# Optimization experiments

Hardware: AMD Instinct MI355X
Metric: run time of the kernel (lower is better)

Reference implementation:

```python
import jax, jax.numpy as jnp
import numpy as np

EPS = 1e-8

def setup_inputs() -> dict:
    key = jax.random.key(0)
    ks = jax.random.split(key, 12)
    bsz, input_dim, output_dim = 65536, 512, 512
    base_mem_size, category_mem_size, mem_dim, n_cat = 100, 5, 64, 35
    def kaiming(k, shape):
        fan_in = shape[-1]
        bound = np.sqrt(6.0 / fan_in)  # kaiming_uniform with a=sqrt(5) default gain approximated by gain=1 uniform: sqrt(6/fan_in)
        return jax.random.uniform(k, shape, jnp.float32, -bound, bound)
    def linear(kw, kb, out_d, in_d):
        bound = 1.0 / np.sqrt(in_d)
        W = jax.random.uniform(kw, (out_d, in_d), jnp.float32, -bound, bound)
        b = jax.random.uniform(kb, (out_d,), jnp.float32, -bound, bound)
        return W, b
    W_base, b_base = linear(ks[0], ks[1], mem_dim, input_dim)
    W_cat, b_cat = linear(ks[2], ks[3], mem_dim, input_dim)
    W_out, b_out = linear(ks[4], ks[5], output_dim, 2 * mem_dim)
    base_keys = kaiming(ks[6], (base_mem_size, mem_dim))
    base_vals = kaiming(ks[7], (base_mem_size, mem_dim))
    cat_keys = kaiming(ks[8], (n_cat, category_mem_size, mem_dim))
    cat_vals = kaiming(ks[9], (n_cat, category_mem_size, mem_dim))
    query = jax.random.normal(ks[10], (bsz, input_dim), jnp.float32)
    category_idxs = jax.random.randint(ks[11], (bsz,), 0, n_cat)
    return {"query": query, "category_idxs": category_idxs,
            "W_base": W_base, "b_base": b_base, "W_cat": W_cat, "b_cat": b_cat,
            "base_keys": base_keys, "base_vals": base_vals,
            "cat_keys": cat_keys, "cat_vals": cat_vals,
            "W_out": W_out, "b_out": b_out}

def _l2norm(x, axis=-1):
    n = jnp.sqrt(jnp.sum(x * x, axis=axis, keepdims=True))
    return x / jnp.maximum(n, EPS)

def reference(query, category_idxs, W_base, b_base, W_cat, b_cat,
              base_keys, base_vals, cat_keys, cat_vals, W_out, b_out):
    # --- base memory lookup (cosine sim + softmax + weighted sum) ---
    base_query = query @ W_base.T + b_base                      # [b, d]
    base_sims = _l2norm(base_query) @ _l2norm(base_keys).T      # [b, M]
    base_attn = jax.nn.softmax(base_sims, axis=-1)
    base_lookup = base_attn @ base_vals                         # [b, d]
    # --- category memory lookup (gather + dot + softmax + weighted sum) ---
    cat_query = query @ W_cat.T + b_cat                         # [b, d]
    ck = cat_keys[category_idxs]                                # [b, K, d]
    cv = cat_vals[category_idxs]                                # [b, K, d]
    cat_sims = jnp.einsum('bd,bkd->bk', cat_query, ck)          # [b, K]
    cat_attn = jax.nn.softmax(cat_sims, axis=-1)
    cat_lookup = jnp.einsum('bk,bkd->bd', cat_attn, cv)         # [b, d]
    # --- output projection ---
    combined = jnp.concatenate([base_lookup, cat_lookup], axis=1)  # [b, 2d]
    return combined @ W_out.T + b_out                           # [b, out]
```

## Files before the change

kernel.cpp:

```cpp
#include <hip/hip_runtime.h>

typedef _Float16 f16;
typedef _Float16 f16x4 __attribute__((ext_vector_type(4)));
typedef _Float16 f16x8 __attribute__((ext_vector_type(8)));
typedef float    f32x4 __attribute__((ext_vector_type(4)));

#define BATCH 65536
#define INDIM 512
#define MD    64
#define MSZ   100
#define NCAT  35
#define CKSZ  5
#define ODIM  512
#define N1    256
#define K2    128
#define NSLOT (NCAT*CKSZ)
#define RBS   232

static __device__ __forceinline__ f32x4 mfma16(f16x4 a, f16x4 b, f32x4 c) {
  return __builtin_amdgcn_mfma_f32_16x16x16f16(a, b, c, 0, 0, 0);
}

__global__ __launch_bounds__(256) void k_prep(
    const float* __restrict__ Wb, const float* __restrict__ bb,
    const float* __restrict__ Wc, const float* __restrict__ bc,
    const float* __restrict__ keys, const float* __restrict__ bvals,
    const float* __restrict__ cvals, const float* __restrict__ Wo,
    f16* __restrict__ B1, float* __restrict__ bias1,
    f16* __restrict__ B2p, f16* __restrict__ C2cat) {
  int id = blockIdx.x * 256 + threadIdx.x;
  if (id < N1 * INDIM) {
    int k = id & (INDIM - 1);
    int n = id >> 9;
    float v = 0.f;
    if (n < 64) v = Wb[n * INDIM + k];
    else if (n < 128) v = Wc[(n - 64) * INDIM + k];
    else if (n < 128 + MSZ) {
      int m = n - 128;
      float s = 0.f;
      for (int d = 0; d < MD; d++) { float kv = keys[m * MD + d]; s += kv * kv; }
      float dn = fmaxf(sqrtf(s), 1e-8f);
      float a = 0.f;
      for (int d = 0; d < MD; d++) a += Wb[d * INDIM + k] * keys[m * MD + d];
      v = a / dn;
    }
    B1[n * INDIM + k] = (f16)v;
    if (k == 0) {
      float bv = 0.f;
      if (n < 64) bv = bb[n];
      else if (n < 128) bv = bc[n - 64];
      else if (n < 128 + MSZ) {
        int m = n - 128;
        float s = 0.f;
        for (int d = 0; d < MD; d++) { float kv = keys[m * MD + d]; s += kv * kv; }
        float dn = fmaxf(sqrtf(s), 1e-8f);
        float a = 0.f;
        for (int d = 0; d < MD; d++) a += bb[d] * keys[m * MD + d];
        bv = a / dn;
      }
      bias1[n] = bv;
    }
  } else if (id < N1 * INDIM + 16384) {
    int q2 = id - N1 * INDIM;
    int l = q2 & 63, otile = q2 >> 9;
    int o = otile * 16 + (l & 15);
    int kkb = ((q2 >> 6) & 7) * 16 + 4 * (l >> 4);
    float v0 = 0.f, v1 = 0.f, v2 = 0.f, v3 = 0.f;
    if (kkb < MSZ) {
      for (int d = 0; d < MD; d++) {
        float w = Wo[o * 128 + d];
        v0 += bvals[(kkb + 0) * MD + d] * w;
        v1 += bvals[(kkb + 1) * MD + d] * w;
        v2 += bvals[(kkb + 2) * MD + d] * w;
        v3 += bvals[(kkb + 3) * MD + d] * w;
      }
    }
    f16x4 o4; o4[0] = (f16)v0; o4[1] = (f16)v1; o4[2] = (f16)v2; o4[3] = (f16)v3;
    *(f16x4*)(B2p + (size_t)q2 * 4) = o4;
  } else if (id < N1 * INDIM + 16384 + NSLOT * ODIM) {
    int id3 = id - N1 * INDIM - 16384;
    int s = id3 >> 9, o = id3 & 511;
    float a = 0.f;
    for (int d = 0; d < MD; d++) a += cvals[s * MD + d] * Wo[o * 128 + 64 + d];
    C2cat[(size_t)s * ODIM + o] = (f16)a;
  }
}

__global__ __launch_bounds__(512) void k_g1mid(const float* __restrict__ q,
    const f16* __restrict__ B1, const float* __restrict__ bias1,
    const int* __restrict__ cidx, const float* __restrict__ catk,
    f16* __restrict__ A2, float* __restrict__ cwg, int* __restrict__ csg) {
  __shared__ __align__(16) char smem[128 * RBS * 2];
  f16 (*Al)[72] = (f16(*)[72])smem;
  f16 (*Bl)[72] = (f16(*)[72])(smem + 18432);
  f16 (*rb)[RBS] = (f16(*)[RBS])smem;

  const int tid = threadIdx.x;
  const int lane = tid & 63, wid = tid >> 6;
  const int wm = wid & 1, wn = wid >> 1;
  const int row0 = blockIdx.x * 128;
  const int l15 = lane & 15, l4 = lane >> 4;
  f32x4 acc[4][4];
#pragma unroll
  for (int i = 0; i < 4; i++)
#pragma unroll
    for (int j = 0; j < 4; j++) acc[i][j] = (f32x4){0.f, 0.f, 0.f, 0.f};

  const int arow = tid >> 2, aseg = tid & 3;
  const int brow = tid >> 1, bh = tid & 1;

  for (int k0 = 0; k0 < INDIM; k0 += 64) {
    const float* qp = q + (size_t)(row0 + arow) * INDIM + k0 + aseg * 16;
    f32x4 a0 = *(const f32x4*)qp;
    f32x4 a1 = *(const f32x4*)(qp + 4);
    f32x4 a2 = *(const f32x4*)(qp + 8);
    f32x4 a3 = *(const f32x4*)(qp + 12);
    f16x8 av0, av1;
#pragma unroll
    for (int i = 0; i < 4; i++) { av0[i] = (f16)a0[i]; av0[4 + i] = (f16)a1[i]; }
#pragma unroll
    for (int i = 0; i < 4; i++) { av1[i] = (f16)a2[i]; av1[4 + i] = (f16)a3[i]; }
    const f16* bp = B1 + brow * INDIM + k0 + bh * 32;
    f16x8 bv0 = *(const f16x8*)(bp);
    f16x8 bv1 = *(const f16x8*)(bp + 8);
    f16x8 bv2 = *(const f16x8*)(bp + 16);
    f16x8 bv3 = *(const f16x8*)(bp + 24);
    __syncthreads();
    *(f16x8*)&Al[arow][aseg * 16]     = av0;
    *(f16x8*)&Al[arow][aseg * 16 + 8] = av1;
    *(f16x8*)&Bl[brow][bh * 32]      = bv0;
    *(f16x8*)&Bl[brow][bh * 32 + 8]  = bv1;
    *(f16x8*)&Bl[brow][bh * 32 + 16] = bv2;
    *(f16x8*)&Bl[brow][bh * 32 + 24] = bv3;
    __syncthreads();
#pragma unroll
    for (int kk = 0; kk < 4; kk++) {
      const int kc = kk * 16 + 4 * l4;
      f16x4 af[4], bf[4];
#pragma unroll
      for (int mi = 0; mi < 4; mi++) af[mi] = *(const f16x4*)&Al[wm * 64 + mi * 16 + l15][kc];
#pragma unroll
      for (int ni = 0; ni < 4; ni++) bf[ni] = *(const f16x4*)&Bl[wn * 64 + ni * 16 + l15][kc];
#pragma unroll
      for (int mi = 0; mi < 4; mi++)
#pragma unroll
        for (int ni = 0; ni < 4; ni++)
          acc[mi][ni] = mfma16(af[mi], bf[ni], acc[mi][ni]);
    }
  }
  __syncthreads();

#pragma unroll
  for (int ni = 0; ni < 4; ni++) {
    const int col = wn * 64 + ni * 16 + l15;
    const float bs = bias1[col];
    if (col < RBS) {
#pragma unroll
      for (int mi = 0; mi < 4; mi++) {
        const int r = wm * 64 + mi * 16 + 4 * l4;
#pragma unroll
        for (int j = 0; j < 4; j++)
          rb[r + j][col] = (f16)(acc[mi][ni][j] + bs);
      }
    }
  }
  __syncthreads();

  {
    const int row = tid >> 2, s = tid & 3;
    f16x8 v0 = *(const f16x8*)&rb[row][s * 16];
    f16x8 v1 = *(const f16x8*)&rb[row][s * 16 + 8];
    float nb = 0.f;
#pragma unroll
    for (int i = 0; i < 8; i++) { float x = (float)v0[i]; nb += x * x; }
#pragma unroll
    for (int i = 0; i < 8; i++) { float x = (float)v1[i]; nb += x * x; }
    nb += __shfl_xor(nb, 1, 64);
    nb += __shfl_xor(nb, 2, 64);
    const float rinv = 1.f / fmaxf(sqrtf(nb), 1e-8f);

    float sv[25];
#pragma unroll
    for (int i = 0; i < 25; i++)
      sv[i] = (float)rb[row][128 + s * 25 + i] * rinv;
    float mx = sv[0];
#pragma unroll
    for (int i = 1; i < 25; i++) mx = fmaxf(mx, sv[i]);
    mx = fmaxf(mx, __shfl_xor(mx, 1, 64));
    mx = fmaxf(mx, __shfl_xor(mx, 2, 64));
    float es = 0.f;
#pragma unroll
    for (int i = 0; i < 25; i++) { sv[i] = __expf(sv[i] - mx); es += sv[i]; }
    es += __shfl_xor(es, 1, 64);
    es += __shfl_xor(es, 2, 64);
    const float isum = 1.f / es;

    const int ci = cidx[row0 + row];
    const float* kp = catk + (size_t)ci * (CKSZ * MD) + s * 16;
    f16x8 c0 = *(const f16x8*)&rb[row][64 + s * 16];
    f16x8 c1 = *(const f16x8*)&rb[row][64 + s * 16 + 8];
    float cqf[16];
#pragma unroll
    for (int i = 0; i < 8; i++) { cqf[i] = (float)c0[i]; cqf[8 + i] = (float)c1[i]; }
    float t[5];
#pragma unroll
    for (int sl = 0; sl < 5; sl++) {
      f32x4 k0 = *(const f32x4*)(kp + sl * MD);
      f32x4 k1 = *(const f32x4*)(kp + sl * MD + 4);
      f32x4 k2 = *(const f32x4*)(kp + sl * MD + 8);
      f32x4 k3 = *(const f32x4*)(kp + sl * MD + 12);
      float a = 0.f;
#pragma unroll
      for (int i = 0; i < 4; i++) a += cqf[i] * k0[i];
#pragma unroll
      for (int i = 0; i < 4; i++) a += cqf[4 + i] * k1[i];
#pragma unroll
      for (int i = 0; i < 4; i++) a += cqf[8 + i] * k2[i];
#pragma unroll
      for (int i = 0; i < 4; i++) a += cqf[12 + i] * k3[i];
      a += __shfl_xor(a, 1, 64);
      a += __shfl_xor(a, 2, 64);
      t[sl] = a;
    }

#pragma unroll
    for (int i = 0; i < 25; i++)
      rb[row][128 + s * 25 + i] = (f16)(sv[i] * isum);

    if (s == 0) {
      float m5 = fmaxf(fmaxf(fmaxf(t[0], t[1]), fmaxf(t[2], t[3])), t[4]);
      float e0 = __expf(t[0] - m5), e1 = __expf(t[1] - m5), e2 = __expf(t[2] - m5),
            e3 = __expf(t[3] - m5), e4 = __expf(t[4] - m5);
      float ics = 1.f / (e0 + e1 + e2 + e3 + e4);
      float* cwr = cwg + (size_t)(row0 + row) * 5;
      cwr[0] = e0 * ics; cwr[1] = e1 * ics; cwr[2] = e2 * ics;
      cwr[3] = e3 * ics; cwr[4] = e4 * ics;
      csg[row0 + row] = ci * CKSZ;
    }
  }
  __syncthreads();

  {
    const int row = tid >> 2, s = tid & 3;
    f16 tmp[32];
#pragma unroll
    for (int i = 0; i < 32; i++) {
      const int k = s * 32 + i;
      tmp[i] = (k < MSZ) ? rb[row][128 + k] : (f16)0.f;
    }
    f16* dst = A2 + (size_t)(row0 + row) * K2 + s * 32;
#pragma unroll
    for (int i = 0; i < 4; i++)
      *(f16x8*)(dst + i * 8) = *(const f16x8*)&tmp[i * 8];
  }
}

__global__ __launch_bounds__(512) void k_gemm2(const f16* __restrict__ A2,
    const f16* __restrict__ B2p, const float* __restrict__ cwg,
    const int* __restrict__ csg, const f16* __restrict__ C2cat,
    const float* __restrict__ bout, float* __restrict__ out) {
  __shared__ f16 As[128][136];
  __shared__ float cws[128][5];
  __shared__ int csi[128];
  const int tid = threadIdx.x;
  const int lane = tid & 63, wid = tid >> 6;
  const int wm = wid & 1, wn = wid >> 1;
  const int l15 = lane & 15, l4 = lane >> 4;
  const int row0 = blockIdx.x * 128;
  const int col0 = blockIdx.y * 256;

  {
    const int r = tid >> 2, seg = tid & 3;
    const f16* src = A2 + (size_t)(row0 + r) * K2 + seg * 32;
#pragma unroll
    for (int i = 0; i < 4; i++)
      *(f16x8*)&As[r][seg * 32 + i * 8] = *(const f16x8*)(src + i * 8);
  }
  if (tid < 128) {
#pragma unroll
    for (int i = 0; i < 5; i++) cws[tid][i] = cwg[(size_t)(row0 + tid) * 5 + i];
    csi[tid] = csg[row0 + tid];
  }
  __syncthreads();

  f32x4 acc[4][4];
#pragma unroll
  for (int i = 0; i < 4; i++)
#pragma unroll
    for (int j = 0; j < 4; j++) acc[i][j] = (f32x4){0.f, 0.f, 0.f, 0.f};

#pragma unroll
  for (int ks = 0; ks < 8; ks++) {
    f16x4 af[4], bf[4];
#pragma unroll
    for (int mi = 0; mi < 4; mi++)
      af[mi] = *(const f16x4*)&As[wm * 64 + mi * 16 + l15][ks * 16 + 4 * l4];
#pragma unroll
    for (int ni = 0; ni < 4; ni++)
      bf[ni] = *(const f16x4*)(B2p +
        (((size_t)(blockIdx.y * 16 + wn * 4 + ni) * 8 + ks) * 64 + lane) * 4);
#pragma unroll
    for (int mi = 0; mi < 4; mi++)
#pragma unroll
      for (int ni = 0; ni < 4; ni++)
        acc[mi][ni] = mfma16(af[mi], bf[ni], acc[mi][ni]);
  }

  float bs[4];
#pragma unroll
  for (int ni = 0; ni < 4; ni++) bs[ni] = bout[col0 + wn * 64 + ni * 16 + l15];
#pragma unroll
  for (int mi = 0; mi < 4; mi++) {
#pragma unroll
    for (int j = 0; j < 4; j++) {
      const int r = wm * 64 + mi * 16 + 4 * l4 + j;
      const int cb = csi[r];
      const float w0 = cws[r][0], w1 = cws[r][1], w2 = cws[r][2],
                  w3 = cws[r][3], w4 = cws[r][4];
      const f16* cp = C2cat + (size_t)cb * ODIM + col0 + wn * 64 + l15;
#pragma unroll
      for (int ni = 0; ni < 4; ni++) {
        const int col = col0 + wn * 64 + ni * 16 + l15;
        const f16* cpn = cp + ni * 16;
        float v = acc[mi][ni][j] + bs[ni];
        v += w0 * (float)cpn[0]
           + w1 * (float)cpn[ODIM]
           + w2 * (float)cpn[2 * ODIM]
           + w3 * (float)cpn[3 * ODIM]
           + w4 * (float)cpn[4 * ODIM];
        out[(size_t)(row0 + r) * ODIM + col] = v;
      }
    }
  }
}

extern "C" void kernel_launch(void* const* d_in, const int* in_sizes, int n_in,
                              void* d_out, int out_size, void* d_ws, size_t ws_size,
                              hipStream_t stream) {
  const float* query = (const float*)d_in[0];
  const int*   cidx  = (const int*)d_in[1];
  const float* Wb    = (const float*)d_in[2];
  const float* bb    = (const float*)d_in[3];
  const float* Wc    = (const float*)d_in[4];
  const float* bc    = (const float*)d_in[5];
  const float* bkeys = (const float*)d_in[6];
  const float* bvals = (const float*)d_in[7];
  const float* ckeys = (const float*)d_in[8];
  const float* cvals = (const float*)d_in[9];
  const float* Wo    = (const float*)d_in[10];
  const float* bo    = (const float*)d_in[11];
  float* out = (float*)d_out;

  char* ws = (char*)d_ws;
  f16*   A2    = (f16*)(ws);
  float* cwg   = (float*)(ws + 16777216);
  int*   csg   = (int*)(ws + 18087936);
  f16*   B1    = (f16*)(ws + 18350080);
  f16*   B2p   = (f16*)(ws + 18612224);
  f16*   C2cat = (f16*)(ws + 18743296);
  float* bias1 = (float*)(ws + 18922496);

  const int prep_ids = N1 * INDIM + 16384 + NSLOT * ODIM;
  k_prep<<<dim3((prep_ids + 255) / 256), 256, 0, stream>>>(
      Wb, bb, Wc, bc, bkeys, bvals, cvals, Wo, B1, bias1, B2p, C2cat);
  k_g1mid<<<dim3(BATCH / 128), 512, 0, stream>>>(
      query, B1, bias1, cidx, ckeys, A2, cwg, csg);
  k_gemm2<<<dim3(BATCH / 128, 2), 512, 0, stream>>>(A2, B2p, cwg, csg, C2cat, bo, out);
}
```

Measured before the change: 107.4 us.

## Store intermediate A2 in MFMA-fragment order and load it directly from global

The mid kernel now writes the attention-weight matrix A2 in a pre-swizzled layout that matches the 16x16x16 MFMA A-fragment order. The second GEMM then reads fragments straight from global memory, with no LDS staging. This removes the shared-memory tile, its fill loop and the LDS reads in the output GEMM. In exchange, the mid kernel's stores become scattered 8-byte writes, and the GEMM issues more global loads per wave.

Result: slower. 130.2 us (+21.3%).

```diff
diff --git a/kernel.cpp b/kernel.cpp
--- a/kernel.cpp
+++ b/kernel.cpp
@@ -89,7 +89,7 @@
 __global__ __launch_bounds__(512) void k_g1mid(const float* __restrict__ q,
     const f16* __restrict__ B1, const float* __restrict__ bias1,
     const int* __restrict__ cidx, const float* __restrict__ catk,
-    f16* __restrict__ A2, float* __restrict__ cwg, int* __restrict__ csg) {
+    f16* __restrict__ A2p, float* __restrict__ cwg, int* __restrict__ csg) {
   __shared__ __align__(16) char smem[128 * RBS * 2];
   f16 (*Al)[72] = (f16(*)[72])smem;
   f16 (*Bl)[72] = (f16(*)[72])(smem + 18432);
@@ -242,24 +242,29 @@
 
   {
     const int row = tid >> 2, s = tid & 3;
-    f16 tmp[32];
-#pragma unroll
-    for (int i = 0; i < 32; i++) {
-      const int k = s * 32 + i;
-      tmp[i] = (k < MSZ) ? rb[row][128 + k] : (f16)0.f;
-    }
-    f16* dst = A2 + (size_t)(row0 + row) * K2 + s * 32;
-#pragma unroll
-    for (int i = 0; i < 4; i++)
-      *(f16x8*)(dst + i * 8) = *(const f16x8*)&tmp[i * 8];
-  }
-}
-
-__global__ __launch_bounds__(512) void k_gemm2(const f16* __restrict__ A2,
+    const int rowtile = (row0 >> 4) + (row >> 4);
+    const int rl = row & 15;
+#pragma unroll
+    for (int t = 0; t < 2; t++) {
+      const int ks2 = s * 2 + t;
+#pragma unroll
+      for (int l4i = 0; l4i < 4; l4i++) {
+        f16x4 v;
+#pragma unroll
+        for (int j = 0; j < 4; j++) {
+          const int k = ks2 * 16 + l4i * 4 + j;
+          v[j] = (k < MSZ) ? rb[row][128 + k] : (f16)0.f;
+        }
+        *(f16x4*)(A2p + ((size_t)(rowtile * 8 + ks2) * 64 + l4i * 16 + rl) * 4) = v;
+      }
+    }
+  }
+}
+
+__global__ __launch_bounds__(512) void k_gemm2(const f16* __restrict__ A2p,
     const f16* __restrict__ B2p, const float* __restrict__ cwg,
     const int* __restrict__ csg, const f16* __restrict__ C2cat,
     const float* __restrict__ bout, float* __restrict__ out) {
-  __shared__ f16 As[128][136];
   __shared__ float cws[128][5];
   __shared__ int csi[128];
   const int tid = threadIdx.x;
@@ -269,13 +274,6 @@
   const int row0 = blockIdx.x * 128;
   const int col0 = blockIdx.y * 256;
 
-  {
-    const int r = tid >> 2, seg = tid & 3;
-    const f16* src = A2 + (size_t)(row0 + r) * K2 + seg * 32;
-#pragma unroll
-    for (int i = 0; i < 4; i++)
-      *(f16x8*)&As[r][seg * 32 + i * 8] = *(const f16x8*)(src + i * 8);
-  }
   if (tid < 128) {
 #pragma unroll
     for (int i = 0; i < 5; i++) cws[tid][i] = cwg[(size_t)(row0 + tid) * 5 + i];
@@ -289,16 +287,18 @@
 #pragma unroll
     for (int j = 0; j < 4; j++) acc[i][j] = (f32x4){0.f, 0.f, 0.f, 0.f};
 
+  const f16* afbase = A2p + ((size_t)(blockIdx.x * 8 + wm * 4) * 8) * 256 + (size_t)lane * 4;
+  const f16* bfbase = B2p + ((size_t)(blockIdx.y * 16 + wn * 4) * 8) * 256 + (size_t)lane * 4;
+
 #pragma unroll
   for (int ks = 0; ks < 8; ks++) {
     f16x4 af[4], bf[4];
 #pragma unroll
     for (int mi = 0; mi < 4; mi++)
-      af[mi] = *(const f16x4*)&As[wm * 64 + mi * 16 + l15][ks * 16 + 4 * l4];
+      af[mi] = *(const f16x4*)(afbase + ((size_t)mi * 8 + ks) * 256);
 #pragma unroll
     for (int ni = 0; ni < 4; ni++)
-      bf[ni] = *(const f16x4*)(B2p +
-        (((size_t)(blockIdx.y * 16 + wn * 4 + ni) * 8 + ks) * 64 + lane) * 4);
+      bf[ni] = *(const f16x4*)(bfbase + ((size_t)ni * 8 + ks) * 256);
 #pragma unroll
     for (int mi = 0; mi < 4; mi++)
 #pragma unroll
@@ -352,7 +352,7 @@
   float* out = (float*)d_out;
 
   char* ws = (char*)d_ws;
-  f16*   A2    = (f16*)(ws);
+  f16*   A2p   = (f16*)(ws);
   float* cwg   = (float*)(ws + 16777216);
   int*   csg   = (int*)(ws + 18087936);
   f16*   B1    = (f16*)(ws + 18350080);
@@ -364,6 +364,6 @@
   k_prep<<<dim3((prep_ids + 255) / 256), 256, 0, stream>>>(
       Wb, bb, Wc, bc, bkeys, bvals, cvals, Wo, B1, bias1, B2p, C2cat);
   k_g1mid<<<dim3(BATCH / 128), 512, 0, stream>>>(
-      query, B1, bias1, cidx, ckeys, A2, cwg, csg);
-  k_gemm2<<<dim3(BATCH / 128, 2), 512, 0, stream>>>(A2, B2p, cwg, csg, C2cat, bo, out);
-}
+      query, B1, bias1, cidx, ckeys, A2p, cwg, csg);
+  k_gemm2<<<dim3(BATCH / 128, 2), 512, 0, stream>>>(A2p, B2p, cwg, csg, C2cat, bo, out);
+}
```

## Pre-pack B1 in MFMA fragment order and load B directly to registers

Applied to the files above, without the earlier changes.

The prep kernel now writes the first-GEMM weight matrix in a fragment-packed layout, so each lane reads its f16x4 MFMA operand straight from global memory (through cache) instead of staging B through LDS. This removes the B tile LDS writes and reads and shrinks the LDS traffic per k-step, at the cost of more global/L2 loads per wave and higher register use (16 f16x4 fragments per step). The bias computation is split into its own id range, and the key-projection loop is vectorised to four outputs per thread.

After: 117.4 us. 9.3% more time.

```diff
diff --git a/kernel.cpp b/kernel.cpp
--- a/kernel.cpp
+++ b/kernel.cpp
@@ -26,42 +26,36 @@
     const float* __restrict__ Wc, const float* __restrict__ bc,
     const float* __restrict__ keys, const float* __restrict__ bvals,
     const float* __restrict__ cvals, const float* __restrict__ Wo,
-    f16* __restrict__ B1, float* __restrict__ bias1,
+    f16* __restrict__ B1p, float* __restrict__ bias1,
     f16* __restrict__ B2p, f16* __restrict__ C2cat) {
   int id = blockIdx.x * 256 + threadIdx.x;
-  if (id < N1 * INDIM) {
-    int k = id & (INDIM - 1);
-    int n = id >> 9;
-    float v = 0.f;
-    if (n < 64) v = Wb[n * INDIM + k];
-    else if (n < 128) v = Wc[(n - 64) * INDIM + k];
-    else if (n < 128 + MSZ) {
+  if (id < 32768) {
+    int l = id & 63, ntile = id >> 11;
+    int n = ntile * 16 + (l & 15);
+    int kb = ((id >> 6) & 31) * 16 + 4 * (l >> 4);
+    float v0 = 0.f, v1 = 0.f, v2 = 0.f, v3 = 0.f;
+    if (n < 64) {
+      const float* w = Wb + n * INDIM + kb;
+      v0 = w[0]; v1 = w[1]; v2 = w[2]; v3 = w[3];
+    } else if (n < 128) {
+      const float* w = Wc + (n - 64) * INDIM + kb;
+      v0 = w[0]; v1 = w[1]; v2 = w[2]; v3 = w[3];
+    } else if (n < 128 + MSZ) {
       int m = n - 128;
-      float s = 0.f;
-      for (int d = 0; d < MD; d++) { float kv = keys[m * MD + d]; s += kv * kv; }
-      float dn = fmaxf(sqrtf(s), 1e-8f);
-      float a = 0.f;
-      for (int d = 0; d < MD; d++) a += Wb[d * INDIM + k] * keys[m * MD + d];
-      v = a / dn;
-    }
-    B1[n * INDIM + k] = (f16)v;
-    if (k == 0) {
-      float bv = 0.f;
-      if (n < 64) bv = bb[n];
-      else if (n < 128) bv = bc[n - 64];
-      else if (n < 128 + MSZ) {
-        int m = n - 128;
-        float s = 0.f;
-        for (int d = 0; d < MD; d++) { float kv = keys[m * MD + d]; s += kv * kv; }
-        float dn = fmaxf(sqrtf(s), 1e-8f);
-        float a = 0.f;
-        for (int d = 0; d < MD; d++) a += bb[d] * keys[m * MD + d];
-        bv = a / dn;
+      float ss = 0.f;
+      for (int d = 0; d < MD; d++) { float kv = keys[m * MD + d]; ss += kv * kv; }
+      float rin = 1.f / fmaxf(sqrtf(ss), 1e-8f);
+      for (int d = 0; d < MD; d++) {
+        float kd = keys[m * MD + d];
+        const float* wr = Wb + d * INDIM + kb;
+        v0 += wr[0] * kd; v1 += wr[1] * kd; v2 += wr[2] * kd; v3 += wr[3] * kd;
       }
-      bias1[n] = bv;
-    }
-  } else if (id < N1 * INDIM + 16384) {
-    int q2 = id - N1 * INDIM;
+      v0 *= rin; v1 *= rin; v2 *= rin; v3 *= rin;
+    }
+    f16x4 o; o[0] = (f16)v0; o[1] = (f16)v1; o[2] = (f16)v2; o[3] = (f16)v3;
+    *(f16x4*)(B1p + (size_t)id * 4) = o;
+  } else if (id < 49152) {
+    int q2 = id - 32768;
     int l = q2 & 63, otile = q2 >> 9;
     int o = otile * 16 + (l & 15);
     int kkb = ((q2 >> 6) & 7) * 16 + 4 * (l >> 4);
@@ -77,22 +71,36 @@
     }
     f16x4 o4; o4[0] = (f16)v0; o4[1] = (f16)v1; o4[2] = (f16)v2; o4[3] = (f16)v3;
     *(f16x4*)(B2p + (size_t)q2 * 4) = o4;
-  } else if (id < N1 * INDIM + 16384 + NSLOT * ODIM) {
-    int id3 = id - N1 * INDIM - 16384;
+  } else if (id < 138752) {
+    int id3 = id - 49152;
     int s = id3 >> 9, o = id3 & 511;
     float a = 0.f;
     for (int d = 0; d < MD; d++) a += cvals[s * MD + d] * Wo[o * 128 + 64 + d];
     C2cat[(size_t)s * ODIM + o] = (f16)a;
+  } else if (id < 139008) {
+    int n = id - 138752;
+    float bv = 0.f;
+    if (n < 64) bv = bb[n];
+    else if (n < 128) bv = bc[n - 64];
+    else if (n < 128 + MSZ) {
+      int m = n - 128;
+      float ss = 0.f;
+      for (int d = 0; d < MD; d++) { float kv = keys[m * MD + d]; ss += kv * kv; }
+      float rin = 1.f / fmaxf(sqrtf(ss), 1e-8f);
+      float a = 0.f;
+      for (int d = 0; d < MD; d++) a += bb[d] * keys[m * MD + d];
+      bv = a * rin;
+    }
+    bias1[n] = bv;
   }
 }
 
 __global__ __launch_bounds__(512) void k_g1mid(const float* __restrict__ q,
-    const f16* __restrict__ B1, const float* __restrict__ bias1,
+    const f16* __restrict__ B1p, const float* __restrict__ bias1,
     const int* __restrict__ cidx, const float* __restrict__ catk,
     f16* __restrict__ A2, float* __restrict__ cwg, int* __restrict__ csg) {
   __shared__ __align__(16) char smem[128 * RBS * 2];
   f16 (*Al)[72] = (f16(*)[72])smem;
-  f16 (*Bl)[72] = (f16(*)[72])(smem + 18432);
   f16 (*rb)[RBS] = (f16(*)[RBS])smem;
 
   const int tid = threadIdx.x;
@@ -107,7 +115,7 @@
     for (int j = 0; j < 4; j++) acc[i][j] = (f32x4){0.f, 0.f, 0.f, 0.f};
 
   const int arow = tid >> 2, aseg = tid & 3;
-  const int brow = tid >> 1, bh = tid & 1;
+  const f16* bfbase = B1p + ((size_t)(wn * 4) * 32) * 256 + (size_t)lane * 4;
 
   for (int k0 = 0; k0 < INDIM; k0 += 64) {
     const float* qp = q + (size_t)(row0 + arow) * INDIM + k0 + aseg * 16;
@@ -115,37 +123,33 @@
     f32x4 a1 = *(const f32x4*)(qp + 4);
     f32x4 a2 = *(const f32x4*)(qp + 8);
     f32x4 a3 = *(const f32x4*)(qp + 12);
+    f16x4 bf[4][4];
+    const int ksb = k0 >> 4;
+#pragma unroll
+    for (int kk = 0; kk < 4; kk++)
+#pragma unroll
+      for (int ni = 0; ni < 4; ni++)
+        bf[kk][ni] = *(const f16x4*)(bfbase + ((size_t)ni * 32 + ksb + kk) * 256);
     f16x8 av0, av1;
 #pragma unroll
     for (int i = 0; i < 4; i++) { av0[i] = (f16)a0[i]; av0[4 + i] = (f16)a1[i]; }
 #pragma unroll
     for (int i = 0; i < 4; i++) { av1[i] = (f16)a2[i]; av1[4 + i] = (f16)a3[i]; }
-    const f16* bp = B1 + brow * INDIM + k0 + bh * 32;
-    f16x8 bv0 = *(const f16x8*)(bp);
-    f16x8 bv1 = *(const f16x8*)(bp + 8);
-    f16x8 bv2 = *(const f16x8*)(bp + 16);
-    f16x8 bv3 = *(const f16x8*)(bp + 24);
     __syncthreads();
     *(f16x8*)&Al[arow][aseg * 16]     = av0;
     *(f16x8*)&Al[arow][aseg * 16 + 8] = av1;
-    *(f16x8*)&Bl[brow][bh * 32]      = bv0;
-    *(f16x8*)&Bl[brow][bh * 32 + 8]  = bv1;
-    *(f16x8*)&Bl[brow][bh * 32 + 16] = bv2;
-    *(f16x8*)&Bl[brow][bh * 32 + 24] = bv3;
     __syncthreads();
 #pragma unroll
     for (int kk = 0; kk < 4; kk++) {
       const int kc = kk * 16 + 4 * l4;
-      f16x4 af[4], bf[4];
+      f16x4 af[4];
 #pragma unroll
       for (int mi = 0; mi < 4; mi++) af[mi] = *(const f16x4*)&Al[wm * 64 + mi * 16 + l15][kc];
 #pragma unroll
-      for (int ni = 0; ni < 4; ni++) bf[ni] = *(const f16x4*)&Bl[wn * 64 + ni * 16 + l15][kc];
-#pragma unroll
       for (int mi = 0; mi < 4; mi++)
 #pragma unroll
         for (int ni = 0; ni < 4; ni++)
-          acc[mi][ni] = mfma16(af[mi], bf[ni], acc[mi][ni]);
+          acc[mi][ni] = mfma16(af[mi], bf[kk][ni], acc[mi][ni]);
     }
   }
   __syncthreads();
@@ -355,15 +359,14 @@
   f16*   A2    = (f16*)(ws);
   float* cwg   = (float*)(ws + 16777216);
   int*   csg   = (int*)(ws + 18087936);
-  f16*   B1    = (f16*)(ws + 18350080);
+  f16*   B1p   = (f16*)(ws + 18350080);
   f16*   B2p   = (f16*)(ws + 18612224);
   f16*   C2cat = (f16*)(ws + 18743296);
   float* bias1 = (float*)(ws + 18922496);
 
-  const int prep_ids = N1 * INDIM + 16384 + NSLOT * ODIM;
-  k_prep<<<dim3((prep_ids + 255) / 256), 256, 0, stream>>>(
-      Wb, bb, Wc, bc, bkeys, bvals, cvals, Wo, B1, bias1, B2p, C2cat);
+  k_prep<<<dim3((139008 + 255) / 256), 256, 0, stream>>>(
+      Wb, bb, Wc, bc, bkeys, bvals, cvals, Wo, B1p, bias1, B2p, C2cat);
   k_g1mid<<<dim3(BATCH / 128), 512, 0, stream>>>(
-      query, B1, bias1, cidx, ckeys, A2, cwg, csg);
+      query, B1p, bias1, cidx, ckeys, A2, cwg, csg);
   k_gemm2<<<dim3(BATCH / 128, 2), 512, 0, stream>>>(A2, B2p, cwg, csg, C2cat, bo, out);
 }
```
